# Optimization experiments

Measured on AMD Instinct MI355X. Metric: run time of the kernel, lower is better.

Reference implementation:

```python
import jax, jax.numpy as jnp
import numpy as np

N = 50000
E = 1600000
VOCAB = 1000
EMB = 128
HID = 128
OUT = 128


def setup_inputs() -> dict:
    key = jax.random.key(0)
    ks = jax.random.split(key, 8)
    labels = jax.random.randint(ks[0], (N,), 0, VOCAB)
    edge_index = jax.random.randint(ks[1], (2, E), 0, N)
    weight = jax.random.uniform(ks[2], (E,), dtype=jnp.float32)
    emb_table = jax.random.normal(ks[3], (VOCAB, EMB), dtype=jnp.float32) * 0.02
    W1 = jax.random.normal(ks[4], (EMB, HID), dtype=jnp.float32) * (1.0 / np.sqrt(EMB))
    b1 = jnp.zeros((HID,), dtype=jnp.float32)
    W2 = jax.random.normal(ks[5], (HID, OUT), dtype=jnp.float32) * (1.0 / np.sqrt(HID))
    b2 = jnp.zeros((OUT,), dtype=jnp.float32)
    return {"labels": labels, "edge_index": edge_index, "weight": weight,
            "emb_table": emb_table, "W1": W1, "b1": b1, "W2": W2, "b2": b2}


def _gcn_conv(x, src, dst, ew, W, b, n_nodes):
    # PyG GCNConv: linear transform, then symmetric-normalized weighted aggregation.
    x = x @ W  # [N, F_out]
    deg = jax.ops.segment_sum(ew, dst, num_segments=n_nodes)  # weighted in-degree (incl. self loops)
    dinv = jnp.where(deg > 0, jax.lax.rsqrt(deg), 0.0)
    norm = dinv[src] * ew * dinv[dst]  # [E_tot]
    msg = x[src] * norm[:, None]  # gather + scale
    out = jax.ops.segment_sum(msg, dst, num_segments=n_nodes)  # scatter-add
    return out + b


def reference(labels, edge_index, weight, emb_table, W1, b1, W2, b2):
    n_nodes = emb_table.shape[0] if False else labels.shape[0]
    # add self loops with weight 1.0 (GCNConv default add_self_loops=True)
    loop = jnp.arange(n_nodes, dtype=edge_index.dtype)
    src = jnp.concatenate([edge_index[0], loop])
    dst = jnp.concatenate([edge_index[1], loop])
    ew = jnp.concatenate([weight.astype(jnp.float32), jnp.ones((n_nodes,), jnp.float32)])

    x = emb_table[labels]  # embedding lookup [N, EMB]
    x = _gcn_conv(x, src, dst, ew, W1, b1, n_nodes)
    x = jax.nn.relu(x)
    x = _gcn_conv(x, src, dst, ew, W2, b2, n_nodes)
    return x
```

## Files before the change

### kernel.cpp

```cpp
#include <hip/hip_runtime.h>
#include <hip/hip_fp16.h>


#define CHUNKS 256
#define BSTAGE 2816

__global__ __launch_bounds__(1024) void hist_kernel(const int* __restrict__ dst,
                                                    int* __restrict__ hist,
                                                    int e, int chunk, int nb) {
  __shared__ unsigned lh[1024];
  int b = blockIdx.x, t = threadIdx.x;
  lh[t] = 0;
  __syncthreads();
  int start = b * chunk, end = min(e, start + chunk);
  for (int i = start + t; i < end; i += 1024) atomicAdd(&lh[dst[i] >> 6], 1u);
  __syncthreads();
  if (t < nb) hist[(size_t)t * CHUNKS + b] = (int)lh[t];
}

__global__ __launch_bounds__(256) void colscan_kernel(const int* __restrict__ hist,
                                                      int* __restrict__ off,
                                                      int* __restrict__ tot,
                                                      int nb, int bact) {
  int k = (blockIdx.x * 256 + threadIdx.x) >> 6;
  int lane = threadIdx.x & 63;
  if (k >= nb) return;
  int carry = 0;
  for (int r = 0; r < CHUNKS / 64; ++r) {
    int b = r * 64 + lane;
    int h = (b < bact) ? hist[(size_t)k * CHUNKS + b] : 0;
    int x = h;
#pragma unroll
    for (int d = 1; d < 64; d <<= 1) {
      int tt = __shfl_up(x, d, 64);
      if (lane >= d) x += tt;
    }
    if (b < bact) off[(size_t)k * CHUNKS + b] = carry + x - h;
    carry += __shfl(x, 63, 64);
  }
  if (lane == 0) tot[k] = carry;
}

__global__ __launch_bounds__(1024) void ebase_kernel(const int* __restrict__ tot,
                                                     int* __restrict__ ebase, int nb) {
  __shared__ int wsum[16];
  int t = threadIdx.x, lane = t & 63, wv = t >> 6;
  int v = (t < nb) ? tot[t] : 0;
  int x = v;
#pragma unroll
  for (int d = 1; d < 64; d <<= 1) {
    int tt = __shfl_up(x, d, 64);
    if (lane >= d) x += tt;
  }
  if (lane == 63) wsum[wv] = x;
  __syncthreads();
  int o = 0;
#pragma unroll
  for (int w = 0; w < 16; ++w) o += (w < wv) ? wsum[w] : 0;
  int excl = x - v + o;
  if (t < nb) ebase[t] = excl;
  if (t == nb - 1) ebase[nb] = excl + v;
}

__global__ __launch_bounds__(1024) void scatter_kernel(
    const int* __restrict__ src, const int* __restrict__ dst,
    const float* __restrict__ w, const int* __restrict__ labels,
    const int* __restrict__ off, const int* __restrict__ ebase,
    int2* __restrict__ brec, int e, int chunk, int nb) {
  __shared__ unsigned bincnt[1024];
  __shared__ int gbase[1024];
  int b = blockIdx.x, t = threadIdx.x;
  bincnt[t] = 0;
  if (t < nb) gbase[t] = ebase[t] + off[(size_t)t * CHUNKS + b];
  __syncthreads();
  int start = b * chunk, end = min(e, start + chunk);
  int s[7], d[7], lb[7], ps[7];
  float wv[7];
#pragma unroll
  for (int u = 0; u < 7; ++u) {
    int i = start + u * 1024 + t;
    bool ok = i < end;
    s[u] = ok ? src[i] : 0;
    d[u] = ok ? dst[i] : 0;
    wv[u] = ok ? w[i] : 0.f;
  }
#pragma unroll
  for (int u = 0; u < 7; ++u) lb[u] = labels[s[u]];
#pragma unroll
  for (int u = 0; u < 7; ++u) ps[u] = gbase[d[u] >> 6];
#pragma unroll
  for (int u = 0; u < 7; ++u) {
    int i = start + u * 1024 + t;
    if (i < end) {
      int k = d[u] >> 6;
      unsigned lr = atomicAdd(&bincnt[k], 1u);
      unsigned rx = (unsigned)s[u] | ((unsigned)(d[u] & 63) << 16) |
                    ((unsigned)lb[u] << 22);
      brec[ps[u] + (int)lr] = make_int2((int)rx, __float_as_int(wv[u]));
    }
  }
}

__global__ __launch_bounds__(256) void bsort_kernel(const int2* __restrict__ brec,
                                                    const int* __restrict__ ebase,
                                                    int2* __restrict__ csr,
                                                    int* __restrict__ rs,
                                                    float* __restrict__ dinv, int n) {
  __shared__ int2 stage[BSTAGE];
  __shared__ unsigned h64[64];
  __shared__ unsigned cur[64];
  __shared__ float rsum[64];
  int k = blockIdx.x, t = threadIdx.x;
  int e0 = ebase[k], e1 = ebase[k + 1], cnt = e1 - e0;
  if (t < 64) { h64[t] = 0; rsum[t] = 0.f; }
  __syncthreads();
  bool fits = (cnt <= BSTAGE);
  for (int i = t; i < cnt; i += 256) {
    int2 r = brec[e0 + i];
    if (fits) stage[i] = r;
    unsigned dl = ((unsigned)r.x >> 16) & 63u;
    atomicAdd(&h64[dl], 1u);
    atomicAdd(&rsum[dl], __int_as_float(r.y));
  }
  __syncthreads();
  if (t < 64) {
    int hv = (int)h64[t];
    int x = hv;
#pragma unroll
    for (int d = 1; d < 64; d <<= 1) {
      int tt = __shfl_up(x, d, 64);
      if (t >= d) x += tt;
    }
    int ex = x - hv;
    cur[t] = (unsigned)(e0 + ex);
    int v = k * 64 + t;
    if (v <= n) rs[v] = e0 + ex;
    if (v < n) dinv[v] = rsqrtf(1.0f + rsum[t]);
  }
  __syncthreads();
  for (int i = t; i < cnt; i += 256) {
    int2 r = fits ? stage[i] : brec[e0 + i];
    unsigned rx = (unsigned)r.x;
    int dl = (int)((rx >> 16) & 63u);
    int pos = (int)atomicAdd(&cur[dl], 1u);
    csr[pos] = make_int2((int)((rx & 0xffffu) | ((rx >> 22) << 16)), r.y);
  }
}

__global__ void temb_kernel(const float* __restrict__ emb, const float* __restrict__ W1,
                            __half* __restrict__ temb) {
  int r = blockIdx.x, j = threadIdx.x;
  __shared__ float xs[128];
  xs[j] = emb[r * 128 + j];
  __syncthreads();
  float acc = 0.f;
#pragma unroll 8
  for (int k = 0; k < 128; ++k) acc = fmaf(xs[k], W1[k * 128 + j], acc);
  temb[r * 128 + j] = __float2half_rn(acc);
}

__device__ __forceinline__ void unpack4(float2 raw, float2& a, float2& b) {
  union { float f; __half2 h; } u0, u1;
  u0.f = raw.x;
  u1.f = raw.y;
  a = __half22float2(u0.h);
  b = __half22float2(u1.h);
}

__global__ __launch_bounds__(256) void agg1_kernel(
    const int* __restrict__ rs, const int2* __restrict__ csr,
    const float* __restrict__ dinv, const int* __restrict__ labels,
    const __half* __restrict__ temb, const float* __restrict__ b1,
    __half* __restrict__ out1, int n) {
  int wid = (blockIdx.x * blockDim.x + threadIdx.x) >> 6;
  int lane = threadIdx.x & 63;
  if (wid >= n) return;
  int half = lane >> 5, fl = lane & 31;
  float di = dinv[wid];
  float acc0, acc1, acc2, acc3;
  {
    int selfrow = labels[wid];
    float2 raw = ((const float2*)(temb + (size_t)selfrow * 128))[fl];
    float2 a, b;
    unpack4(raw, a, b);
    float ss = half ? 0.f : di;
    acc0 = a.x * ss; acc1 = a.y * ss; acc2 = b.x * ss; acc3 = b.y * ss;
  }
  int r1v = rs[wid + 1];
  for (int base = rs[wid]; base < r1v; base += 64) {
    int s = 0;
    float v = 0.f;
    if (base + lane < r1v) {
      int2 c = csr[base + lane];
      s = c.x;
      v = __int_as_float(c.y) * dinv[c.x & 0xffff];
    }
    int nb = min(64, r1v - base);
    int j = 0;
    for (; j + 16 <= nb; j += 16) {
#pragma unroll
      for (int u = 0; u < 8; ++u) {
        int jj = j + 2 * u + half;
        int sj = __shfl(s, jj, 64);
        float vj = __shfl(v, jj, 64);
        float2 raw = ((const float2*)(temb + (size_t)(sj >> 16) * 128))[fl];
        float2 a, b;
        unpack4(raw, a, b);
        acc0 = fmaf(a.x, vj, acc0); acc1 = fmaf(a.y, vj, acc1);
        acc2 = fmaf(b.x, vj, acc2); acc3 = fmaf(b.y, vj, acc3);
      }
    }
    for (; j + 2 <= nb; j += 2) {
      int jj = j + half;
      int sj = __shfl(s, jj, 64);
      float vj = __shfl(v, jj, 64);
      float2 raw = ((const float2*)(temb + (size_t)(sj >> 16) * 128))[fl];
      float2 a, b;
      unpack4(raw, a, b);
      acc0 = fmaf(a.x, vj, acc0); acc1 = fmaf(a.y, vj, acc1);
      acc2 = fmaf(b.x, vj, acc2); acc3 = fmaf(b.y, vj, acc3);
    }
    if (j < nb) {
      int sj = __shfl(s, j, 64);
      float vj0 = __shfl(v, j, 64);
      float vj = half ? 0.f : vj0;
      float2 raw = ((const float2*)(temb + (size_t)(sj >> 16) * 128))[fl];
      float2 a, b;
      unpack4(raw, a, b);
      acc0 = fmaf(a.x, vj, acc0); acc1 = fmaf(a.y, vj, acc1);
      acc2 = fmaf(b.x, vj, acc2); acc3 = fmaf(b.y, vj, acc3);
    }
  }
  acc0 += __shfl_xor(acc0, 32, 64);
  acc1 += __shfl_xor(acc1, 32, 64);
  acc2 += __shfl_xor(acc2, 32, 64);
  acc3 += __shfl_xor(acc3, 32, 64);
  if (half == 0) {
    float4 b4 = ((const float4*)b1)[fl];
    acc0 = fmaxf(fmaf(acc0, di, b4.x), 0.f);
    acc1 = fmaxf(fmaf(acc1, di, b4.y), 0.f);
    acc2 = fmaxf(fmaf(acc2, di, b4.z), 0.f);
    acc3 = fmaxf(fmaf(acc3, di, b4.w), 0.f);
    union { float2 f2; __half2 h2[2]; } o;
    o.h2[0] = __float22half2_rn(make_float2(acc0, acc1));
    o.h2[1] = __float22half2_rn(make_float2(acc2, acc3));
    ((float2*)(out1 + (size_t)wid * 128))[fl] = o.f2;
  }
}

__global__ __launch_bounds__(256) void agg2_kernel(
    const int* __restrict__ rs, const int2* __restrict__ csr,
    const float* __restrict__ dinv, const __half* __restrict__ h,
    float* __restrict__ out, int n) {
  int wid = (blockIdx.x * blockDim.x + threadIdx.x) >> 6;
  int lane = threadIdx.x & 63;
  if (wid >= n) return;
  int half = lane >> 5, fl = lane & 31;
  float di = dinv[wid];
  float acc0, acc1, acc2, acc3;
  {
    float2 raw = ((const float2*)(h + (size_t)wid * 128))[fl];
    float2 a, b;
    unpack4(raw, a, b);
    float ss = half ? 0.f : di;
    acc0 = a.x * ss; acc1 = a.y * ss; acc2 = b.x * ss; acc3 = b.y * ss;
  }
  int r1v = rs[wid + 1];
  for (int base = rs[wid]; base < r1v; base += 64) {
    int s = 0;
    float v = 0.f;
    if (base + lane < r1v) {
      int2 c = csr[base + lane];
      s = c.x;
      v = __int_as_float(c.y) * dinv[c.x & 0xffff];
    }
    int nb = min(64, r1v - base);
    int j = 0;
    for (; j + 16 <= nb; j += 16) {
#pragma unroll
      for (int u = 0; u < 8; ++u) {
        int jj = j + 2 * u + half;
        int sj = __shfl(s, jj, 64);
        float vj = __shfl(v, jj, 64);
        float2 raw = ((const float2*)(h + (size_t)(sj & 0xffff) * 128))[fl];
        float2 a, b;
        unpack4(raw, a, b);
        acc0 = fmaf(a.x, vj, acc0); acc1 = fmaf(a.y, vj, acc1);
        acc2 = fmaf(b.x, vj, acc2); acc3 = fmaf(b.y, vj, acc3);
      }
    }
    for (; j + 2 <= nb; j += 2) {
      int jj = j + half;
      int sj = __shfl(s, jj, 64);
      float vj = __shfl(v, jj, 64);
      float2 raw = ((const float2*)(h + (size_t)(sj & 0xffff) * 128))[fl];
      float2 a, b;
      unpack4(raw, a, b);
      acc0 = fmaf(a.x, vj, acc0); acc1 = fmaf(a.y, vj, acc1);
      acc2 = fmaf(b.x, vj, acc2); acc3 = fmaf(b.y, vj, acc3);
    }
    if (j < nb) {
      int sj = __shfl(s, j, 64);
      float vj0 = __shfl(v, j, 64);
      float vj = half ? 0.f : vj0;
      float2 raw = ((const float2*)(h + (size_t)(sj & 0xffff) * 128))[fl];
      float2 a, b;
      unpack4(raw, a, b);
      acc0 = fmaf(a.x, vj, acc0); acc1 = fmaf(a.y, vj, acc1);
      acc2 = fmaf(b.x, vj, acc2); acc3 = fmaf(b.y, vj, acc3);
    }
  }
  acc0 += __shfl_xor(acc0, 32, 64);
  acc1 += __shfl_xor(acc1, 32, 64);
  acc2 += __shfl_xor(acc2, 32, 64);
  acc3 += __shfl_xor(acc3, 32, 64);
  if (half == 0) {
    ((float4*)(out + (size_t)wid * 128))[fl] =
        make_float4(acc0 * di, acc1 * di, acc2 * di, acc3 * di);
  }
}

__global__ __launch_bounds__(256) void gemm_bias_kernel(float* __restrict__ y,
                                                        const float* __restrict__ W,
                                                        const float* __restrict__ bias,
                                                        int n) {
  __shared__ float xs[32][128];
  int tid = threadIdx.x;
  int tc = tid & 31;
  int tr = tid >> 5;
  int rb = blockIdx.x * 32;
  {
    const float4* xg = (const float4*)(y + (size_t)rb * 128);
    float4* xls = (float4*)&xs[0][0];
#pragma unroll
    for (int i = 0; i < 4; ++i) {
      int idx = tid + i * 256;
      int row = rb + (idx >> 5);
      float4 val = (row < n) ? xg[idx] : make_float4(0.f, 0.f, 0.f, 0.f);
      xls[idx] = val;
    }
  }
  __syncthreads();
  int j0 = tc * 4;
  float4 b4 = *(const float4*)(bias + j0);
  float acc[4][4];
#pragma unroll
  for (int r = 0; r < 4; ++r) {
    acc[r][0] = b4.x; acc[r][1] = b4.y; acc[r][2] = b4.z; acc[r][3] = b4.w;
  }
#pragma unroll 4
  for (int k = 0; k < 128; ++k) {
    float4 w4 = *(const float4*)(W + k * 128 + j0);
#pragma unroll
    for (int r = 0; r < 4; ++r) {
      float xv = xs[tr * 4 + r][k];
      acc[r][0] = fmaf(xv, w4.x, acc[r][0]);
      acc[r][1] = fmaf(xv, w4.y, acc[r][1]);
      acc[r][2] = fmaf(xv, w4.z, acc[r][2]);
      acc[r][3] = fmaf(xv, w4.w, acc[r][3]);
    }
  }
#pragma unroll
  for (int r = 0; r < 4; ++r) {
    int row = rb + tr * 4 + r;
    if (row < n)
      *(float4*)(y + (size_t)row * 128 + j0) =
          make_float4(acc[r][0], acc[r][1], acc[r][2], acc[r][3]);
  }
}

extern "C" void kernel_launch(void* const* d_in, const int* in_sizes, int n_in,
                              void* d_out, int out_size, void* d_ws, size_t ws_size,
                              hipStream_t stream) {
  const int* labels = (const int*)d_in[0];
  const int* edge_index = (const int*)d_in[1];
  const float* weight = (const float*)d_in[2];
  const float* emb = (const float*)d_in[3];
  const float* W1 = (const float*)d_in[4];
  const float* b1 = (const float*)d_in[5];
  const float* W2 = (const float*)d_in[6];
  const float* b2 = (const float*)d_in[7];

  int n = in_sizes[0];
  int e = in_sizes[1] / 2;
  int vocab = in_sizes[3] / 128;
  const int* srcp = edge_index;
  const int* dstp = edge_index + e;

  int nb = (n + 63) >> 6;
  int chunk = (e + CHUNKS - 1) / CHUNKS;
  int bact = (e + chunk - 1) / chunk;

  float* ws = (float*)d_ws;
  size_t o = 0;
  auto alloc_f = [&](size_t c) { float* p = ws + o; o += (c + 255) & ~(size_t)255; return p; };
  int*    hist  = (int*)alloc_f((size_t)nb * CHUNKS);
  int*    off   = (int*)alloc_f((size_t)nb * CHUNKS);
  int*    tot   = (int*)alloc_f(nb);
  int*    ebase = (int*)alloc_f(nb + 1);
  int2*   brec  = (int2*)alloc_f((size_t)e * 2);
  int*    rs    = (int*)alloc_f(n + 1);
  int2*   csr   = (int2*)alloc_f((size_t)e * 2);
  float*  dinv  = alloc_f(n);
  __half* temb  = (__half*)alloc_f((size_t)vocab * 64);
  __half* out1  = (__half*)alloc_f((size_t)n * 64);
  (void)ws_size;

  dim3 b256(256);
  dim3 b1024(1024);
  int gagg = (int)(((size_t)n * 64 + 255) / 256);

  hist_kernel<<<bact, b1024, 0, stream>>>(dstp, hist, e, chunk, nb);
  colscan_kernel<<<(nb * 64 + 255) / 256, b256, 0, stream>>>(hist, off, tot, nb, bact);
  ebase_kernel<<<1, b1024, 0, stream>>>(tot, ebase, nb);
  scatter_kernel<<<bact, b1024, 0, stream>>>(srcp, dstp, weight, labels, off, ebase,
                                             brec, e, chunk, nb);
  bsort_kernel<<<nb, b256, 0, stream>>>(brec, ebase, csr, rs, dinv, n);
  temb_kernel<<<vocab, 128, 0, stream>>>(emb, W1, temb);
  agg1_kernel<<<gagg, b256, 0, stream>>>(rs, csr, dinv, labels, temb, b1, out1, n);
  agg2_kernel<<<gagg, b256, 0, stream>>>(rs, csr, dinv, out1, (float*)d_out, n);
  gemm_bias_kernel<<<(n + 31) / 32, b256, 0, stream>>>((float*)d_out, W2, b2, n);
}
```

Before: 186.1 us.

## Stage transformed embedding table in LDS for layer-1 aggregation, prescale edge weights

Layer-1 aggregation now copies the vocab-sized transformed embedding table into shared memory, one 64-feature half at a time, and gathers neighbour rows from LDS instead of global memory. It uses a persistent grid of 256 blocks of 512 threads, with 8 lanes per edge slot and a shuffle reduction. A new scale_kernel folds dinv[src] into the CSR edge weights once, so neither aggregation kernel re-gathers dinv per edge. The trade-offs are an extra pass over the CSR, two passes over all edges in layer 1 (one per feature half), and low occupancy from the roughly 144KB LDS slab, with the slab hardcoded to a vocab of 1000.

```diff
diff --git a/kernel.cpp b/kernel.cpp
--- a/kernel.cpp
+++ b/kernel.cpp
@@ -4,6 +4,7 @@
 
 #define CHUNKS 256
 #define BSTAGE 2816
+#define SLABSTRIDE 72
 
 __global__ __launch_bounds__(1024) void hist_kernel(const int* __restrict__ dst,
                                                     int* __restrict__ hist,
@@ -147,8 +148,17 @@
   }
 }
 
+__global__ void scale_kernel(int2* __restrict__ csr, const float* __restrict__ dinv, int e) {
+  int i = blockIdx.x * blockDim.x + threadIdx.x;
+  if (i < e) {
+    int2 c = csr[i];
+    c.y = __float_as_int(__int_as_float(c.y) * dinv[c.x & 0xffff]);
+    csr[i] = c;
+  }
+}
+
 __global__ void temb_kernel(const float* __restrict__ emb, const float* __restrict__ W1,
-                            __half* __restrict__ temb) {
+                            __half* __restrict__ temb2, int vocab) {
   int r = blockIdx.x, j = threadIdx.x;
   __shared__ float xs[128];
   xs[j] = emb[r * 128 + j];
@@ -156,7 +166,77 @@
   float acc = 0.f;
 #pragma unroll 8
   for (int k = 0; k < 128; ++k) acc = fmaf(xs[k], W1[k * 128 + j], acc);
-  temb[r * 128 + j] = __float2half_rn(acc);
+  int p = j >> 6, c = j & 63;
+  temb2[(size_t)p * vocab * 64 + r * 64 + c] = __float2half_rn(acc);
+}
+
+__global__ __launch_bounds__(512) void agg1_kernel(
+    const int* __restrict__ rs, const int2* __restrict__ csr,
+    const float* __restrict__ dinv, const int* __restrict__ labels,
+    const __half* __restrict__ temb2, const float* __restrict__ b1,
+    __half* __restrict__ out1, int n, int vocab) {
+  __shared__ __half slab[1000 * SLABSTRIDE];
+  int t = threadIdx.x;
+  int gw = (blockIdx.x * 512 + t) >> 6;
+  int lane = t & 63;
+  int g = lane >> 3, li = lane & 7;
+  for (int p = 0; p < 2; ++p) {
+    __syncthreads();
+    {
+      const float4* srcp = (const float4*)(temb2 + (size_t)p * vocab * 64);
+      for (int i = t; i < vocab * 8; i += 512) {
+        int row = i >> 3, c8 = i & 7;
+        *(float4*)&slab[row * SLABSTRIDE + c8 * 8] = srcp[i];
+      }
+    }
+    __syncthreads();
+    for (int wid = gw; wid < n; wid += 2048) {
+      int r0 = rs[wid], r1 = rs[wid + 1];
+      float acc[8] = {0.f, 0.f, 0.f, 0.f, 0.f, 0.f, 0.f, 0.f};
+      for (int k = r0; k < r1; k += 8) {
+        int kk = k + g;
+        int2 c = csr[kk];
+        bool ok = kk < r1;
+        float vj = ok ? __int_as_float(c.y) : 0.f;
+        int lab = ok ? (int)(((unsigned)c.x) >> 16) : 0;
+        float4 raw = *(const float4*)&slab[lab * SLABSTRIDE + li * 8];
+        __half2* hp = (__half2*)&raw;
+#pragma unroll
+        for (int q = 0; q < 4; ++q) {
+          float2 f = __half22float2(hp[q]);
+          acc[2 * q] = fmaf(f.x, vj, acc[2 * q]);
+          acc[2 * q + 1] = fmaf(f.y, vj, acc[2 * q + 1]);
+        }
+      }
+#pragma unroll
+      for (int d = 8; d < 64; d <<= 1) {
+#pragma unroll
+        for (int q = 0; q < 8; ++q) acc[q] += __shfl_xor(acc[q], d, 64);
+      }
+      if (lane < 8) {
+        float di = dinv[wid];
+        int lab0 = labels[wid];
+        float4 sraw = *(const float4*)&slab[lab0 * SLABSTRIDE + lane * 8];
+        __half2* sp = (__half2*)&sraw;
+        float4 bA = *(const float4*)(b1 + p * 64 + lane * 8);
+        float4 bB = *(const float4*)(b1 + p * 64 + lane * 8 + 4);
+        float bb[8] = {bA.x, bA.y, bA.z, bA.w, bB.x, bB.y, bB.z, bB.w};
+        float o[8];
+#pragma unroll
+        for (int q = 0; q < 4; ++q) {
+          float2 sf = __half22float2(sp[q]);
+          o[2 * q] = fmaxf(fmaf(acc[2 * q] + sf.x * di, di, bb[2 * q]), 0.f);
+          o[2 * q + 1] =
+              fmaxf(fmaf(acc[2 * q + 1] + sf.y * di, di, bb[2 * q + 1]), 0.f);
+        }
+        union { float4 f4; __half2 h2[4]; } u;
+#pragma unroll
+        for (int q = 0; q < 4; ++q)
+          u.h2[q] = __float22half2_rn(make_float2(o[2 * q], o[2 * q + 1]));
+        *(float4*)(out1 + (size_t)wid * 128 + p * 64 + lane * 8) = u.f4;
+      }
+    }
+  }
 }
 
 __device__ __forceinline__ void unpack4(float2 raw, float2& a, float2& b) {
@@ -165,87 +245,6 @@
   u1.f = raw.y;
   a = __half22float2(u0.h);
   b = __half22float2(u1.h);
-}
-
-__global__ __launch_bounds__(256) void agg1_kernel(
-    const int* __restrict__ rs, const int2* __restrict__ csr,
-    const float* __restrict__ dinv, const int* __restrict__ labels,
-    const __half* __restrict__ temb, const float* __restrict__ b1,
-    __half* __restrict__ out1, int n) {
-  int wid = (blockIdx.x * blockDim.x + threadIdx.x) >> 6;
-  int lane = threadIdx.x & 63;
-  if (wid >= n) return;
-  int half = lane >> 5, fl = lane & 31;
-  float di = dinv[wid];
-  float acc0, acc1, acc2, acc3;
-  {
-    int selfrow = labels[wid];
-    float2 raw = ((const float2*)(temb + (size_t)selfrow * 128))[fl];
-    float2 a, b;
-    unpack4(raw, a, b);
-    float ss = half ? 0.f : di;
-    acc0 = a.x * ss; acc1 = a.y * ss; acc2 = b.x * ss; acc3 = b.y * ss;
-  }
-  int r1v = rs[wid + 1];
-  for (int base = rs[wid]; base < r1v; base += 64) {
-    int s = 0;
-    float v = 0.f;
-    if (base + lane < r1v) {
-      int2 c = csr[base + lane];
-      s = c.x;
-      v = __int_as_float(c.y) * dinv[c.x & 0xffff];
-    }
-    int nb = min(64, r1v - base);
-    int j = 0;
-    for (; j + 16 <= nb; j += 16) {
-#pragma unroll
-      for (int u = 0; u < 8; ++u) {
-        int jj = j + 2 * u + half;
-        int sj = __shfl(s, jj, 64);
-        float vj = __shfl(v, jj, 64);
-        float2 raw = ((const float2*)(temb + (size_t)(sj >> 16) * 128))[fl];
-        float2 a, b;
-        unpack4(raw, a, b);
-        acc0 = fmaf(a.x, vj, acc0); acc1 = fmaf(a.y, vj, acc1);
-        acc2 = fmaf(b.x, vj, acc2); acc3 = fmaf(b.y, vj, acc3);
-      }
-    }
-    for (; j + 2 <= nb; j += 2) {
-      int jj = j + half;
-      int sj = __shfl(s, jj, 64);
-      float vj = __shfl(v, jj, 64);
-      float2 raw = ((const float2*)(temb + (size_t)(sj >> 16) * 128))[fl];
-      float2 a, b;
-      unpack4(raw, a, b);
-      acc0 = fmaf(a.x, vj, acc0); acc1 = fmaf(a.y, vj, acc1);
-      acc2 = fmaf(b.x, vj, acc2); acc3 = fmaf(b.y, vj, acc3);
-    }
-    if (j < nb) {
-      int sj = __shfl(s, j, 64);
-      float vj0 = __shfl(v, j, 64);
-      float vj = half ? 0.f : vj0;
-      float2 raw = ((const float2*)(temb + (size_t)(sj >> 16) * 128))[fl];
-      float2 a, b;
-      unpack4(raw, a, b);
-      acc0 = fmaf(a.x, vj, acc0); acc1 = fmaf(a.y, vj, acc1);
-      acc2 = fmaf(b.x, vj, acc2); acc3 = fmaf(b.y, vj, acc3);
-    }
-  }
-  acc0 += __shfl_xor(acc0, 32, 64);
-  acc1 += __shfl_xor(acc1, 32, 64);
-  acc2 += __shfl_xor(acc2, 32, 64);
-  acc3 += __shfl_xor(acc3, 32, 64);
-  if (half == 0) {
-    float4 b4 = ((const float4*)b1)[fl];
-    acc0 = fmaxf(fmaf(acc0, di, b4.x), 0.f);
-    acc1 = fmaxf(fmaf(acc1, di, b4.y), 0.f);
-    acc2 = fmaxf(fmaf(acc2, di, b4.z), 0.f);
-    acc3 = fmaxf(fmaf(acc3, di, b4.w), 0.f);
-    union { float2 f2; __half2 h2[2]; } o;
-    o.h2[0] = __float22half2_rn(make_float2(acc0, acc1));
-    o.h2[1] = __float22half2_rn(make_float2(acc2, acc3));
-    ((float2*)(out1 + (size_t)wid * 128))[fl] = o.f2;
-  }
 }
 
 __global__ __launch_bounds__(256) void agg2_kernel(
@@ -272,7 +271,7 @@
     if (base + lane < r1v) {
       int2 c = csr[base + lane];
       s = c.x;
-      v = __int_as_float(c.y) * dinv[c.x & 0xffff];
+      v = __int_as_float(c.y);
     }
     int nb = min(64, r1v - base);
     int j = 0;
@@ -400,9 +399,9 @@
   int*    ebase = (int*)alloc_f(nb + 1);
   int2*   brec  = (int2*)alloc_f((size_t)e * 2);
   int*    rs    = (int*)alloc_f(n + 1);
-  int2*   csr   = (int2*)alloc_f((size_t)e * 2);
+  int2*   csr   = (int2*)alloc_f((size_t)e * 2 + 16);
   float*  dinv  = alloc_f(n);
-  __half* temb  = (__half*)alloc_f((size_t)vocab * 64);
+  __half* temb2 = (__half*)alloc_f((size_t)vocab * 64);
   __half* out1  = (__half*)alloc_f((size_t)n * 64);
   (void)ws_size;
 
@@ -416,8 +415,10 @@
   scatter_kernel<<<bact, b1024, 0, stream>>>(srcp, dstp, weight, labels, off, ebase,
                                              brec, e, chunk, nb);
   bsort_kernel<<<nb, b256, 0, stream>>>(brec, ebase, csr, rs, dinv, n);
-  temb_kernel<<<vocab, 128, 0, stream>>>(emb, W1, temb);
-  agg1_kernel<<<gagg, b256, 0, stream>>>(rs, csr, dinv, labels, temb, b1, out1, n);
+  scale_kernel<<<(e + 255) / 256, b256, 0, stream>>>(csr, dinv, e);
+  temb_kernel<<<vocab, 128, 0, stream>>>(emb, W1, temb2, vocab);
+  agg1_kernel<<<256, 512, 0, stream>>>(rs, csr, dinv, labels, temb2, b1, out1, n,
+                                       vocab);
   agg2_kernel<<<gagg, b256, 0, stream>>>(rs, csr, dinv, out1, (float*)d_out, n);
   gemm_bias_kernel<<<(n + 31) / 32, b256, 0, stream>>>((float*)d_out, W2, b2, n);
 }
```

Result: slower. 250.6 us (+34.7%).
